# Performance work log

Measured on AMD Instinct MI355X. Metric: run time of the kernel, lower is better.

Reference implementation:

```python
import jax, jax.numpy as jnp
import numpy as np
import math

B, S, F, H, C = 64, 64, 4096, 1024, 31


def setup_inputs() -> dict:
    key = jax.random.key(0)
    ks = jax.random.split(key, 10)
    inp = {
        "x": jax.random.normal(ks[0], (B, S, F), dtype=jnp.float32),
        "h0": jax.random.normal(ks[1], (B, H), dtype=jnp.float32),
        "Wxe": jax.random.normal(ks[2], (F, H), dtype=jnp.float32) / math.sqrt(F),
        "bxe": jnp.zeros((H,), jnp.float32),
        "Wep": jax.random.normal(ks[3], (H, C), dtype=jnp.float32) / math.sqrt(H),
        "bep": jnp.zeros((C,), jnp.float32),
        "Whr": jax.random.normal(ks[4], (H, H), dtype=jnp.float32) / math.sqrt(H),
        "bhr": jnp.zeros((H,), jnp.float32),
        "Wx0r": jax.random.normal(ks[5], (H, H), dtype=jnp.float32) / math.sqrt(H),
        "bx0r": jnp.zeros((H,), jnp.float32),
        "Wxtz": jax.random.normal(ks[6], (H, H), dtype=jnp.float32) / math.sqrt(H),
        "bxtz": jnp.zeros((H,), jnp.float32),
        "Wx0z": jax.random.normal(ks[7], (H, H), dtype=jnp.float32) / math.sqrt(H),
        "bx0z": jnp.zeros((H,), jnp.float32),
        "Wxth1": jax.random.normal(ks[8], (H, H), dtype=jnp.float32) / math.sqrt(H),
        "bxth1": jnp.zeros((H,), jnp.float32),
        "Wh1h1": jax.random.normal(ks[9], (H, H), dtype=jnp.float32) / math.sqrt(H),
        "bh1h1": jnp.zeros((H,), jnp.float32),
    }
    return inp


def reference(x, h0, Wxe, bxe, Wep, bep, Whr, bhr, Wx0r, bx0r,
              Wxtz, bxtz, Wx0z, bx0z, Wxth1, bxth1, Wh1h1, bh1h1):
    # x: (B, S, F); h0: (B, H)
    steps = x.shape[1]
    x0 = x[:, -1]                                            # current information

    # Input-dependent projections are independent of the recurrence -> batch them.
    xtes = jax.nn.relu(jnp.einsum('bsf,fh->bsh', x, Wxe) + bxe)   # (B,S,H)
    x0e = jax.nn.relu(x0 @ Wxe + bxe)                             # (B,H), constant over steps
    ptes = jnp.einsum('bsh,hc->bsc', xtes, Wep) + bep             # (B,S,C)
    p0e = x0e @ Wep + bep                                         # (B,C)

    x0r = x0e @ Wx0r + bx0r                                       # (B,H) step-invariant
    x0z = x0e @ Wx0z + bx0z
    xtz_all = jnp.einsum('bsh,hg->bsg', xtes, Wxtz) + bxtz        # (B,S,H)
    xth1_all = jnp.einsum('bsh,hg->bsg', xtes, Wxth1) + bxth1     # (B,S,H)

    def step(h, inputs):
        xtz, xth1 = inputs                                        # (B,H) each
        rt = jax.nn.sigmoid(h @ Whr + bhr + x0r)
        zt = jax.nn.sigmoid(xtz + x0z)
        h1_t_1 = h @ Wh1h1 + bh1h1
        ht1 = jnp.tanh(xth1 + rt * h1_t_1)
        ht = (1.0 - zt) * ht1 + zt * h
        return ht, ht

    # scan over time: move step axis to front
    xs = (jnp.swapaxes(xtz_all, 0, 1), jnp.swapaxes(xth1_all, 0, 1))  # (S,B,H)
    _, hts_t = jax.lax.scan(step, h0, xs)
    hts = jnp.swapaxes(hts_t, 0, 1)                               # (B,S,H)

    p0es = jnp.broadcast_to(p0e[:, None, :], (p0e.shape[0], steps, p0e.shape[1]))
    x0es = jnp.broadcast_to(x0e[:, None, :], (x0e.shape[0], steps, x0e.shape[1]))
    return (hts, ptes, p0es, x0es * 1.0, xtes) if False else (hts, ptes, p0es, xtes, x0es)
```

## Files before the change

### kernel.cpp

```cpp
#include <hip/hip_runtime.h>
#include <stdint.h>


using bf16 = __bf16;
typedef __attribute__((ext_vector_type(8))) __bf16 bf16x8;
typedef __attribute__((ext_vector_type(4))) float f32x4;

#define B_DIM 64
#define S_DIM 64
#define F_DIM 4096
#define H_DIM 1024
#define C_DIM 31

__global__ void cast_tag_kernel(const float* __restrict__ x, bf16* __restrict__ xbf,
                                const float* __restrict__ h0, unsigned* __restrict__ hT0) {
  int bx = blockIdx.x;
  if (bx < 8192) {
    int i = bx * 256 + threadIdx.x;
    const float4* p = (const float4*)x + (size_t)i * 2;
    float4 a = p[0], b = p[1];
    bf16x8 v;
    v[0] = (bf16)a.x; v[1] = (bf16)a.y; v[2] = (bf16)a.z; v[3] = (bf16)a.w;
    v[4] = (bf16)b.x; v[5] = (bf16)b.y; v[6] = (bf16)b.z; v[7] = (bf16)b.w;
    ((bf16x8*)xbf)[i] = v;
  } else {
    int i = (bx - 8192) * 256 + threadIdx.x;
    union { bf16 b; unsigned short u; } cv;
    cv.b = (bf16)h0[i];
    __hip_atomic_store(hT0 + i, ((unsigned)cv.u << 16), __ATOMIC_RELAXED,
                       __HIP_MEMORY_SCOPE_AGENT);
  }
}

__device__ __forceinline__ void tr64(const float* __restrict__ in, bf16* __restrict__ out,
                                     int R, int C, int tR, int tC) {
  __shared__ float t[64][65];
  int tx = threadIdx.x & 63, ty = threadIdx.x >> 6;
#pragma unroll
  for (int i = 0; i < 16; ++i) {
    int r = tR + i * 4 + ty, c = tC + tx;
    t[i * 4 + ty][tx] = (r < R && c < C) ? in[(size_t)r * C + c] : 0.f;
  }
  __syncthreads();
#pragma unroll
  for (int i = 0; i < 16; ++i) {
    int c = tC + i * 4 + ty, r = tR + tx;
    if (c < C && r < R) out[(size_t)c * R + r] = (bf16)t[tx][i * 4 + ty];
  }
}

__global__ void transpose_all(const float* __restrict__ Wxe, bf16* __restrict__ WxeT,
                              const float* __restrict__ a0, const float* __restrict__ a1,
                              const float* __restrict__ a2, const float* __restrict__ a3,
                              const float* __restrict__ a4, const float* __restrict__ a5,
                              bf16* __restrict__ o0, bf16* __restrict__ o1,
                              bf16* __restrict__ o2,
                              const float* __restrict__ Wep, bf16* __restrict__ WepT) {
  int id = blockIdx.x;
  if (id < 1024) {
    tr64(Wxe, WxeT, 4096, 1024, (id & 63) * 64, (id >> 6) * 64);
  } else if (id < 2560) {
    int q = id - 1024, z = q >> 8, t = q & 255;
    const float* in = z == 0 ? a0 : z == 1 ? a1 : z == 2 ? a2 : z == 3 ? a3 : z == 4 ? a4 : a5;
    bf16* out = (z < 2 ? o0 : z < 4 ? o1 : o2) + (size_t)(z & 1) * 1048576;
    tr64(in, out, 1024, 1024, (t & 15) * 64, (t >> 4) * 64);
  } else {
    tr64(Wep, WepT, 1024, 31, (id - 2560) * 64, 0);
  }
}

template <int MODE>
__launch_bounds__(256, 2)
__global__ void gemm_bt(const bf16* __restrict__ A, const bf16* __restrict__ B,
                        int M, int N, int K, int lda,
                        const float* __restrict__ bias0,
                        const float* __restrict__ bias1,
                        const float* __restrict__ bias2,
                        const float* __restrict__ x0rz,
                        float* __restrict__ outA,
                        float* __restrict__ outB,
                        float* __restrict__ outC,
                        float* __restrict__ outD,
                        bf16* __restrict__ outBf) {
  __shared__ bf16 ldsA[128 * 64];
  __shared__ bf16 ldsB[128 * 64];
  const int tid = threadIdx.x;
  const int lane = tid & 63;
  const int wave = tid >> 6;
  const int quad = lane >> 4;
  const int l15 = lane & 15;
  const int wm = wave & 1, wn = wave >> 1;
  const int m0 = blockIdx.x * 128, n0 = blockIdx.y * 128;
  const int kPer = K / gridDim.z;
  const int k0 = blockIdx.z * kPer;

  f32x4 acc[4][4] = {};

  for (int kc = k0; kc < k0 + kPer; kc += 64) {
#pragma unroll
    for (int i = 0; i < 4; ++i) {
      int qb = i * 256 + wave * 64;
      int q = qb + lane;
      int r = q >> 3, cs = q & 7;
      int c = cs ^ (r & 7);
      int gr = m0 + r; if (gr > M - 1) gr = M - 1;
      __builtin_amdgcn_global_load_lds(
          (const __attribute__((address_space(1))) unsigned int*)(A + (size_t)gr * lda + kc + c * 8),
          (__attribute__((address_space(3))) unsigned int*)(ldsA + (size_t)qb * 8),
          16, 0, 0);
      __builtin_amdgcn_global_load_lds(
          (const __attribute__((address_space(1))) unsigned int*)(B + (size_t)(n0 + r) * K + kc + c * 8),
          (__attribute__((address_space(3))) unsigned int*)(ldsB + (size_t)qb * 8),
          16, 0, 0);
    }
    __syncthreads();
#pragma unroll
    for (int ks = 0; ks < 2; ++ks) {
      bf16x8 af[4], bfr[4];
      int ch = ks * 4 + quad;
#pragma unroll
      for (int t = 0; t < 4; ++t) {
        int ar = wm * 64 + t * 16 + l15;
        af[t] = *(const bf16x8*)(ldsA + ar * 64 + ((ch ^ (ar & 7)) * 8));
        int br = wn * 64 + t * 16 + l15;
        bfr[t] = *(const bf16x8*)(ldsB + br * 64 + ((ch ^ (br & 7)) * 8));
      }
#pragma unroll
      for (int mt = 0; mt < 4; ++mt)
#pragma unroll
        for (int nt = 0; nt < 4; ++nt)
          acc[mt][nt] = __builtin_amdgcn_mfma_f32_16x16x32_bf16(
              af[mt], bfr[nt], acc[mt][nt], 0, 0, 0);
    }
    __syncthreads();
  }

#pragma unroll
  for (int mt = 0; mt < 4; ++mt) {
#pragma unroll
    for (int nt = 0; nt < 4; ++nt) {
#pragma unroll
      for (int i = 0; i < 4; ++i) {
        int m = m0 + wm * 64 + mt * 16 + quad * 4 + i;
        int n = n0 + wn * 64 + nt * 16 + l15;
        if (m >= M) continue;
        float v = acc[mt][nt][i];
        if (MODE == 0) {
          v += bias0[n];
          v = fmaxf(v, 0.f);
          outA[(size_t)m * 1024 + n] = v;
          outBf[(size_t)m * 1024 + n] = (bf16)v;
          if ((m & 63) == 63) {
            size_t base = (size_t)(m >> 6) * 64 * 1024 + n;
            for (int sp = 0; sp < 64; ++sp) outD[base + (size_t)sp * 1024] = v;
          }
        } else if (MODE == 1) {
          if (n < 1024) {
            float z = v + bias0[n] + x0rz[(size_t)(m >> 6) * 2048 + 1024 + n];
            outA[(size_t)m * 1024 + n] = 1.f / (1.f + expf(-z));
          } else if (n < 2048) {
            outB[(size_t)m * 1024 + (n - 1024)] = v + bias1[n - 1024];
          } else if (n < 2048 + C_DIM) {
            float pv = v + bias2[n - 2048];
            outC[(size_t)m * C_DIM + (n - 2048)] = pv;
            if ((m & 63) == 63) {
              size_t base = (size_t)(m >> 6) * 64 * C_DIM + (n - 2048);
              for (int sp = 0; sp < 64; ++sp) outD[base + (size_t)sp * C_DIM] = pv;
            }
          }
        } else {
          if (k0 == 0) v += (n < 1024 ? bias0[n] : bias1[n - 1024]);
          atomicAdd(outA + (size_t)m * 2048 + n, v);
        }
      }
    }
  }
}

#define TAG_OK(v, w) \
  ((((unsigned)(v) & 0xFFFFu) == (w)) & (((unsigned)((v) >> 32) & 0xFFFFu) == (w)))

__launch_bounds__(256, 1)
__global__ void recur_kernel(const bf16* __restrict__ WrecT,
                             const float* __restrict__ bhr,
                             const float* __restrict__ bh1h1,
                             const float* __restrict__ x0rz,
                             const float* __restrict__ ztAll,
                             const float* __restrict__ xth1All,
                             const float* __restrict__ h0,
                             unsigned* hT0,
                             unsigned* hT1,
                             float* __restrict__ hts) {
  __shared__ bf16 ldsA[2][16 * 1024];
  const int tid = threadIdx.x;
  const int lane = tid & 63, wave = tid >> 6;
  const int quad = lane >> 4, l15 = lane & 15;
  const int j = blockIdx.x >> 2;
  const int g = blockIdx.x & 3;
  const int col = j * 64 + wave * 16 + l15;

  bf16x8 wr[32], wh[32];
#pragma unroll
  for (int kb = 0; kb < 32; ++kb) {
    wr[kb] = *(const bf16x8*)(WrecT + (size_t)col * 1024 + kb * 32 + quad * 8);
    wh[kb] = *(const bf16x8*)(WrecT + (size_t)(1024 + col) * 1024 + kb * 32 + quad * 8);
  }
  float hb_ = bh1h1[col];
  float rb[4], hloc[4];
#pragma unroll
  for (int i = 0; i < 4; ++i) {
    int b = g * 16 + quad * 4 + i;
    rb[i] = bhr[col] + x0rz[(size_t)b * 2048 + col];
    hloc[i] = h0[(size_t)b * 1024 + col];
  }

  for (int s = 0; s < 64; ++s) {
    const unsigned want = (unsigned)s;
    const unsigned long long* src =
        (const unsigned long long*)(((s & 1) ? hT1 : hT0) + (size_t)g * 16384);
    float zt[4], xh[4];
#pragma unroll
    for (int i = 0; i < 4; ++i) {
      size_t mrow = ((size_t)(g * 16 + quad * 4 + i) * 64 + s) * 1024 + col;
      zt[i] = ztAll[mrow];
      xh[i] = xth1All[mrow];
    }
    bf16* dstL = ldsA[s & 1];
#pragma unroll
    for (int half = 0; half < 2; ++half) {
      unsigned long long q0[8], q1[8];
#pragma unroll
      for (int r8 = 0; r8 < 8; ++r8) {
        const unsigned long long* p = src + (size_t)(half * 8 + r8) * 512 + tid * 2;
        q0[r8] = __hip_atomic_load(p, __ATOMIC_RELAXED, __HIP_MEMORY_SCOPE_AGENT);
        q1[r8] = __hip_atomic_load(p + 1, __ATOMIC_RELAXED, __HIP_MEMORY_SCOPE_AGENT);
      }
      unsigned miss = 0;
#pragma unroll
      for (int r8 = 0; r8 < 8; ++r8)
        if (!(TAG_OK(q0[r8], want) && TAG_OK(q1[r8], want))) miss |= 1u << r8;
      for (int it = 0; miss && it < (1 << 20); ++it) {
#pragma unroll
        for (int r8 = 0; r8 < 8; ++r8)
          if (miss & (1u << r8)) {
            const unsigned long long* p = src + (size_t)(half * 8 + r8) * 512 + tid * 2;
            unsigned long long a = __hip_atomic_load(p, __ATOMIC_RELAXED, __HIP_MEMORY_SCOPE_AGENT);
            unsigned long long b = __hip_atomic_load(p + 1, __ATOMIC_RELAXED, __HIP_MEMORY_SCOPE_AGENT);
            if (TAG_OK(a, want) && TAG_OK(b, want)) {
              q0[r8] = a; q1[r8] = b;
              miss &= ~(1u << r8);
            }
          }
      }
#pragma unroll
      for (int r8 = 0; r8 < 8; ++r8) {
        int r = half * 8 + r8;
        unsigned d0 = (unsigned)q0[r8], d1 = (unsigned)(q0[r8] >> 32);
        unsigned d2 = (unsigned)q1[r8], d3 = (unsigned)(q1[r8] >> 32);
        unsigned long long pk =
            ((unsigned long long)((d2 >> 16) | (d3 & 0xFFFF0000u)) << 32) |
            ((d0 >> 16) | (d1 & 0xFFFF0000u));
        int cc = ((tid >> 1) & 0x78) | (((tid >> 1) ^ r) & 7);
        *(unsigned long long*)((char*)dstL + r * 2048 + cc * 16 + (tid & 1) * 8) = pk;
      }
    }
    __syncthreads();
    f32x4 racc = {0.f, 0.f, 0.f, 0.f}, hacc = {0.f, 0.f, 0.f, 0.f};
#pragma unroll
    for (int kb = 0; kb < 32; ++kb) {
      int ch = kb * 4 + quad;
      bf16x8 af = *(const bf16x8*)((char*)dstL + l15 * 2048 +
                                   (((ch & 0x78) | ((ch ^ l15) & 7)) * 16));
      racc = __builtin_amdgcn_mfma_f32_16x16x32_bf16(af, wr[kb], racc, 0, 0, 0);
      hacc = __builtin_amdgcn_mfma_f32_16x16x32_bf16(af, wh[kb], hacc, 0, 0, 0);
    }
    unsigned* dst = (s & 1) ? hT0 : hT1;
#pragma unroll
    for (int i = 0; i < 4; ++i) {
      int b = g * 16 + quad * 4 + i;
      size_t mrow = ((size_t)b * 64 + s) * 1024 + col;
      float rt = 1.f / (1.f + expf(-(racc[i] + rb[i])));
      float th = tanhf(xh[i] + rt * (hacc[i] + hb_));
      float hn = (1.f - zt[i]) * th + zt[i] * hloc[i];
      hloc[i] = hn;
      hts[mrow] = hn;
      if (s < 63) {
        union { bf16 b16; unsigned short u; } cv;
        cv.b16 = (bf16)hn;
        __hip_atomic_store(dst + (size_t)b * 1024 + col,
                           ((unsigned)cv.u << 16) | (unsigned)(s + 1),
                           __ATOMIC_RELAXED, __HIP_MEMORY_SCOPE_AGENT);
      }
    }
  }
}

extern "C" void kernel_launch(void* const* d_in, const int* in_sizes, int n_in,
                              void* d_out, int out_size, void* d_ws, size_t ws_size,
                              hipStream_t stream) {
  const float* x     = (const float*)d_in[0];
  const float* h0    = (const float*)d_in[1];
  const float* Wxe   = (const float*)d_in[2];
  const float* bxe   = (const float*)d_in[3];
  const float* Wep   = (const float*)d_in[4];
  const float* bep   = (const float*)d_in[5];
  const float* Whr   = (const float*)d_in[6];
  const float* bhr   = (const float*)d_in[7];
  const float* Wx0r  = (const float*)d_in[8];
  const float* bx0r  = (const float*)d_in[9];
  const float* Wxtz  = (const float*)d_in[10];
  const float* bxtz  = (const float*)d_in[11];
  const float* Wx0z  = (const float*)d_in[12];
  const float* bx0z  = (const float*)d_in[13];
  const float* Wxth1 = (const float*)d_in[14];
  const float* bxth1 = (const float*)d_in[15];
  const float* Wh1h1 = (const float*)d_in[16];
  const float* bh1h1 = (const float*)d_in[17];

  float* out   = (float*)d_out;
  float* hts   = out;
  float* ptes  = out + 4194304;
  float* p0es  = out + 4321280;
  float* xtesO = out + 4448256;
  float* x0es  = out + 8642560;

  char* ws = (char*)d_ws;
  size_t off = 0;
  auto alloc = [&](size_t bytes) -> char* {
    char* p = ws + off;
    off += (bytes + 255) & ~(size_t)255;
    return p;
  };
  bf16*  xbf     = (bf16*)alloc(33554432);
  float* ztAll   = (float*)xbf;
  float* xth1All = (float*)((char*)xbf + 16777216);
  bf16*  WxeT    = (bf16*)alloc(8388608);
  bf16*  W2T     = (bf16*)alloc((size_t)2176 * 1024 * 2);
  bf16*  WrecT   = (bf16*)alloc(4194304);
  bf16*  Wx0T    = (bf16*)alloc(4194304);
  bf16*  xtesBf  = (bf16*)alloc(8388608);
  float* x0rz    = (float*)alloc(524288);
  unsigned* hT0  = (unsigned*)alloc(262144);
  unsigned* hT1  = (unsigned*)alloc(262144);

  hipMemsetAsync(W2T, 0, (size_t)2176 * 1024 * 2, stream);
  hipMemsetAsync(x0rz, 0, 524288, stream);

  dim3 tb(256);
  cast_tag_kernel<<<8448, tb, 0, stream>>>(x, xbf, h0, hT0);
  transpose_all<<<2576, tb, 0, stream>>>(Wxe, WxeT,
                                         Whr, Wh1h1, Wxtz, Wxth1, Wx0r, Wx0z,
                                         WrecT, W2T, Wx0T,
                                         Wep, W2T + 2048 * 1024);

  gemm_bt<0><<<dim3(32, 8), tb, 0, stream>>>(xbf, WxeT, 4096, 1024, 4096, 4096,
                                             bxe, nullptr, nullptr, nullptr,
                                             xtesO, nullptr, nullptr, x0es, xtesBf);
  gemm_bt<2><<<dim3(1, 16, 4), tb, 0, stream>>>(xtesBf + 63 * 1024, Wx0T, 64, 2048, 1024, 65536,
                                                bx0r, bx0z, nullptr, nullptr,
                                                x0rz, nullptr, nullptr, nullptr, nullptr);
  gemm_bt<1><<<dim3(32, 17), tb, 0, stream>>>(xtesBf, W2T, 4096, 2176, 1024, 1024,
                                              bxtz, bxth1, bep, x0rz,
                                              ztAll, xth1All, ptes, p0es, nullptr);

  recur_kernel<<<64, tb, 0, stream>>>(WrecT, bhr, bh1h1, x0rz, ztAll, xth1All,
                                      h0, hT0, hT1, hts);
}
```

Baseline: 607.3 us.

## Streamline recurrence polling, split MFMA chains, fast math, separate x0es broadcast

The recurrent kernel now issues all 16 tagged h-row loads up front, before the zt/xth1 loads, and then spins in a single retry loop. The old scheme polled in two halves with per-row retry. The MFMA k-loop is split into two independent accumulator chains to shorten dependency latency. Sigmoid and tanh use __expf and rcp intrinsics. The next-step h stores are issued before the hts stores to shorten the critical path. The x0es broadcast is moved out of the GEMM epilogue into a separate coalesced kernel, at the cost of an extra launch and slightly lower transcendental precision.

Result: slower. 634.8 us (+4.5%).

```diff
diff --git a/kernel.cpp b/kernel.cpp
--- a/kernel.cpp
+++ b/kernel.cpp
@@ -67,6 +67,14 @@
   } else {
     tr64(Wep, WepT, 1024, 31, (id - 2560) * 64, 0);
   }
+}
+
+__global__ void bcast_x0es(const float* __restrict__ xtesO, float* __restrict__ x0es) {
+  int b = blockIdx.x >> 4, c = blockIdx.x & 15;
+  float4 v = ((const float4*)(xtesO + ((size_t)b * 64 + 63) * 1024))[threadIdx.x];
+  float4* dst = (float4*)(x0es + (size_t)b * 65536 + (size_t)c * 4096) + threadIdx.x;
+#pragma unroll
+  for (int i = 0; i < 4; ++i) dst[i * 256] = v;
 }
 
 template <int MODE>
@@ -150,14 +158,11 @@
           v = fmaxf(v, 0.f);
           outA[(size_t)m * 1024 + n] = v;
           outBf[(size_t)m * 1024 + n] = (bf16)v;
-          if ((m & 63) == 63) {
-            size_t base = (size_t)(m >> 6) * 64 * 1024 + n;
-            for (int sp = 0; sp < 64; ++sp) outD[base + (size_t)sp * 1024] = v;
-          }
         } else if (MODE == 1) {
           if (n < 1024) {
             float z = v + bias0[n] + x0rz[(size_t)(m >> 6) * 2048 + 1024 + n];
-            outA[(size_t)m * 1024 + n] = 1.f / (1.f + expf(-z));
+            outA[(size_t)m * 1024 + n] =
+                __builtin_amdgcn_rcpf(1.f + __expf(-z));
           } else if (n < 2048) {
             outB[(size_t)m * 1024 + (n - 1024)] = v + bias1[n - 1024];
           } else if (n < 2048 + C_DIM) {
@@ -214,10 +219,22 @@
     hloc[i] = h0[(size_t)b * 1024 + col];
   }
 
+  const int off0 = ((quad ^ (l15 & 7)) * 16);
+  const int off1 = (((4 + quad) ^ (l15 & 7)) * 16);
+
   for (int s = 0; s < 64; ++s) {
     const unsigned want = (unsigned)s;
-    const unsigned long long* src =
-        (const unsigned long long*)(((s & 1) ? hT1 : hT0) + (size_t)g * 16384);
+    const unsigned long long* __restrict__ src =
+        (const unsigned long long*)(((s & 1) ? hT1 : hT0) + (size_t)g * 16384) + tid * 2;
+
+    unsigned long long qa[16], qb[16];
+#pragma unroll
+    for (int r = 0; r < 16; ++r) {
+      qa[r] = __hip_atomic_load(src + (size_t)r * 512, __ATOMIC_RELAXED,
+                                __HIP_MEMORY_SCOPE_AGENT);
+      qb[r] = __hip_atomic_load(src + (size_t)r * 512 + 1, __ATOMIC_RELAXED,
+                                __HIP_MEMORY_SCOPE_AGENT);
+    }
     float zt[4], xh[4];
 #pragma unroll
     for (int i = 0; i < 4; ++i) {
@@ -225,72 +242,73 @@
       zt[i] = ztAll[mrow];
       xh[i] = xth1All[mrow];
     }
+    for (int it = 0; ; ++it) {
+      unsigned miss = 0;
+#pragma unroll
+      for (int r = 0; r < 16; ++r)
+        if (!(TAG_OK(qa[r], want) & TAG_OK(qb[r], want))) miss |= 1u << r;
+      if (!miss || it > (1 << 17)) break;
+#pragma unroll
+      for (int r = 0; r < 16; ++r) {
+        qa[r] = __hip_atomic_load(src + (size_t)r * 512, __ATOMIC_RELAXED,
+                                  __HIP_MEMORY_SCOPE_AGENT);
+        qb[r] = __hip_atomic_load(src + (size_t)r * 512 + 1, __ATOMIC_RELAXED,
+                                  __HIP_MEMORY_SCOPE_AGENT);
+      }
+    }
     bf16* dstL = ldsA[s & 1];
 #pragma unroll
-    for (int half = 0; half < 2; ++half) {
-      unsigned long long q0[8], q1[8];
-#pragma unroll
-      for (int r8 = 0; r8 < 8; ++r8) {
-        const unsigned long long* p = src + (size_t)(half * 8 + r8) * 512 + tid * 2;
-        q0[r8] = __hip_atomic_load(p, __ATOMIC_RELAXED, __HIP_MEMORY_SCOPE_AGENT);
-        q1[r8] = __hip_atomic_load(p + 1, __ATOMIC_RELAXED, __HIP_MEMORY_SCOPE_AGENT);
-      }
-      unsigned miss = 0;
-#pragma unroll
-      for (int r8 = 0; r8 < 8; ++r8)
-        if (!(TAG_OK(q0[r8], want) && TAG_OK(q1[r8], want))) miss |= 1u << r8;
-      for (int it = 0; miss && it < (1 << 20); ++it) {
-#pragma unroll
-        for (int r8 = 0; r8 < 8; ++r8)
-          if (miss & (1u << r8)) {
-            const unsigned long long* p = src + (size_t)(half * 8 + r8) * 512 + tid * 2;
-            unsigned long long a = __hip_atomic_load(p, __ATOMIC_RELAXED, __HIP_MEMORY_SCOPE_AGENT);
-            unsigned long long b = __hip_atomic_load(p + 1, __ATOMIC_RELAXED, __HIP_MEMORY_SCOPE_AGENT);
-            if (TAG_OK(a, want) && TAG_OK(b, want)) {
-              q0[r8] = a; q1[r8] = b;
-              miss &= ~(1u << r8);
-            }
-          }
-      }
-#pragma unroll
-      for (int r8 = 0; r8 < 8; ++r8) {
-        int r = half * 8 + r8;
-        unsigned d0 = (unsigned)q0[r8], d1 = (unsigned)(q0[r8] >> 32);
-        unsigned d2 = (unsigned)q1[r8], d3 = (unsigned)(q1[r8] >> 32);
-        unsigned long long pk =
-            ((unsigned long long)((d2 >> 16) | (d3 & 0xFFFF0000u)) << 32) |
-            ((d0 >> 16) | (d1 & 0xFFFF0000u));
-        int cc = ((tid >> 1) & 0x78) | (((tid >> 1) ^ r) & 7);
-        *(unsigned long long*)((char*)dstL + r * 2048 + cc * 16 + (tid & 1) * 8) = pk;
-      }
+    for (int r = 0; r < 16; ++r) {
+      unsigned d0 = (unsigned)qa[r], d1 = (unsigned)(qa[r] >> 32);
+      unsigned d2 = (unsigned)qb[r], d3 = (unsigned)(qb[r] >> 32);
+      unsigned long long pk =
+          ((unsigned long long)((d2 >> 16) | (d3 & 0xFFFF0000u)) << 32) |
+          ((d0 >> 16) | (d1 & 0xFFFF0000u));
+      int cc = ((tid >> 1) & 0x78) | (((tid >> 1) ^ r) & 7);
+      *(unsigned long long*)((char*)dstL + r * 2048 + cc * 16 + (tid & 1) * 8) = pk;
     }
     __syncthreads();
-    f32x4 racc = {0.f, 0.f, 0.f, 0.f}, hacc = {0.f, 0.f, 0.f, 0.f};
-#pragma unroll
-    for (int kb = 0; kb < 32; ++kb) {
-      int ch = kb * 4 + quad;
-      bf16x8 af = *(const bf16x8*)((char*)dstL + l15 * 2048 +
-                                   (((ch & 0x78) | ((ch ^ l15) & 7)) * 16));
-      racc = __builtin_amdgcn_mfma_f32_16x16x32_bf16(af, wr[kb], racc, 0, 0, 0);
-      hacc = __builtin_amdgcn_mfma_f32_16x16x32_bf16(af, wh[kb], hacc, 0, 0, 0);
-    }
+
+    f32x4 racc0 = {0.f, 0.f, 0.f, 0.f}, racc1 = {0.f, 0.f, 0.f, 0.f};
+    f32x4 hacc0 = {0.f, 0.f, 0.f, 0.f}, hacc1 = {0.f, 0.f, 0.f, 0.f};
+    const char* baseL = (const char*)dstL + l15 * 2048;
+#pragma unroll
+    for (int kb = 0; kb < 32; kb += 2) {
+      bf16x8 af0 = *(const bf16x8*)(baseL + (kb >> 1) * 128 + off0);
+      bf16x8 af1 = *(const bf16x8*)(baseL + (kb >> 1) * 128 + off1);
+      racc0 = __builtin_amdgcn_mfma_f32_16x16x32_bf16(af0, wr[kb], racc0, 0, 0, 0);
+      hacc0 = __builtin_amdgcn_mfma_f32_16x16x32_bf16(af0, wh[kb], hacc0, 0, 0, 0);
+      racc1 = __builtin_amdgcn_mfma_f32_16x16x32_bf16(af1, wr[kb + 1], racc1, 0, 0, 0);
+      hacc1 = __builtin_amdgcn_mfma_f32_16x16x32_bf16(af1, wh[kb + 1], hacc1, 0, 0, 0);
+    }
+
     unsigned* dst = (s & 1) ? hT0 : hT1;
+    float hn[4];
 #pragma unroll
     for (int i = 0; i < 4; ++i) {
-      int b = g * 16 + quad * 4 + i;
-      size_t mrow = ((size_t)b * 64 + s) * 1024 + col;
-      float rt = 1.f / (1.f + expf(-(racc[i] + rb[i])));
-      float th = tanhf(xh[i] + rt * (hacc[i] + hb_));
-      float hn = (1.f - zt[i]) * th + zt[i] * hloc[i];
-      hloc[i] = hn;
-      hts[mrow] = hn;
-      if (s < 63) {
+      float ra = racc0[i] + racc1[i];
+      float ha = hacc0[i] + hacc1[i];
+      float rt = __builtin_amdgcn_rcpf(1.f + __expf(-(ra + rb[i])));
+      float e2 = __expf(2.f * (xh[i] + rt * (ha + hb_)));
+      float th = 1.f - 2.f * __builtin_amdgcn_rcpf(e2 + 1.f);
+      hn[i] = (1.f - zt[i]) * th + zt[i] * hloc[i];
+      hloc[i] = hn[i];
+    }
+    if (s < 63) {
+#pragma unroll
+      for (int i = 0; i < 4; ++i) {
+        int b = g * 16 + quad * 4 + i;
         union { bf16 b16; unsigned short u; } cv;
-        cv.b16 = (bf16)hn;
+        cv.b16 = (bf16)hn[i];
         __hip_atomic_store(dst + (size_t)b * 1024 + col,
                            ((unsigned)cv.u << 16) | (unsigned)(s + 1),
                            __ATOMIC_RELAXED, __HIP_MEMORY_SCOPE_AGENT);
       }
+    }
+#pragma unroll
+    for (int i = 0; i < 4; ++i) {
+      size_t mrow = ((size_t)(g * 16 + quad * 4 + i) * 64 + s) * 1024 + col;
+      hts[mrow] = hn[i];
     }
   }
 }
@@ -355,7 +373,8 @@
 
   gemm_bt<0><<<dim3(32, 8), tb, 0, stream>>>(xbf, WxeT, 4096, 1024, 4096, 4096,
                                              bxe, nullptr, nullptr, nullptr,
-                                             xtesO, nullptr, nullptr, x0es, xtesBf);
+                                             xtesO, nullptr, nullptr, nullptr, xtesBf);
+  bcast_x0es<<<1024, tb, 0, stream>>>(xtesO, x0es);
   gemm_bt<2><<<dim3(1, 16, 4), tb, 0, stream>>>(xtesBf + 63 * 1024, Wx0T, 64, 2048, 1024, 65536,
                                                 bx0r, bx0z, nullptr, nullptr,
                                                 x0rz, nullptr, nullptr, nullptr, nullptr);
```
